# Kernel optimization log

Measured on AMD Instinct MI355X. Metric: run time of the kernel, lower is better.

Reference implementation:

```python
import jax, jax.numpy as jnp
import numpy as np

NUM_HEADS = 8
KERNEL = 7  # odd, dilation = 1


def _neighbor_indices(n, k):
    # NATTEN semantics: window start clamped so the kxk window stays inside [0, n)
    r = k // 2
    starts = jnp.clip(jnp.arange(n) - r, 0, n - k)  # [n]
    return starts[:, None] + jnp.arange(k)[None, :]  # [n, k]


def setup_inputs() -> dict:
    key = jax.random.key(0)
    k1, k2, k3, k4 = jax.random.split(key, 4)
    B, H, W, C = 2, 56, 56, 256
    return {
        "x": jax.random.normal(k1, (B, H, W, C), dtype=jnp.float32),
        "w_qk": jax.random.normal(k2, (2 * C, C), dtype=jnp.float32) * 0.02,
        "w_v": jax.random.normal(k3, (C, C), dtype=jnp.float32) * 0.02,
        "w_proj": jax.random.normal(k4, (C, C), dtype=jnp.float32) * 0.02,
        "b_proj": jnp.zeros((C,), dtype=jnp.float32),
    }


def reference(x, w_qk, w_v, w_proj, b_proj):
    B, H, W, C = x.shape
    NH, K = NUM_HEADS, KERNEL
    HD = C // NH
    scale = HD ** -0.5

    # qk / v projections (torch Linear: y = x @ W.T)
    qk = (x @ w_qk.T).reshape(B, H, W, 2, NH, HD)
    q = jnp.moveaxis(qk[:, :, :, 0], 3, 1) * scale  # [B, NH, H, W, HD]
    k = jnp.moveaxis(qk[:, :, :, 1], 3, 1)          # [B, NH, H, W, HD]
    v = jnp.moveaxis((x @ w_v.T).reshape(B, H, W, NH, HD), 3, 1)  # [B, NH, H, W, HD]

    idx_h = _neighbor_indices(H, K)  # [H, K]
    idx_w = _neighbor_indices(W, K)  # [W, K]
    ih = idx_h[:, None, :, None]  # [H, 1, K, 1]
    iw = idx_w[None, :, None, :]  # [1, W, 1, K]

    # Gather per-pixel neighborhoods: [B, NH, H, W, K, K, HD]
    k_nb = k[:, :, ih, iw, :]
    v_nb = v[:, :, ih, iw, :]

    # windowed QK^T -> [B, NH, H, W, K*K]
    attn = jnp.einsum('bnijf,bnijpqf->bnijpq', q, k_nb).reshape(B, NH, H, W, K * K)
    attn = jax.nn.softmax(attn, axis=-1)

    # windowed AV -> [B, NH, H, W, HD]
    out = jnp.einsum('bnijk,bnijkf->bnijf', attn, v_nb.reshape(B, NH, H, W, K * K, HD))

    out = jnp.moveaxis(out, 1, 3).reshape(B, H, W, C)
    out = out @ w_proj.T + b_proj
    return out, attn
```

## Files before the change

### kernel.cpp

```cpp
#include <hip/hip_runtime.h>
#include <math.h>

#define Bb   2
#define Hh   56
#define Ww   56
#define Cc   256
#define NHh  8
#define HDd  32
#define KK   7
#define HWsz (Hh*Ww)
#define Mtot (Bb*Hh*Ww)

typedef __bf16 bf16x8 __attribute__((ext_vector_type(8)));
typedef __bf16 bf16x4 __attribute__((ext_vector_type(4)));
typedef float  f32x4  __attribute__((ext_vector_type(4)));

__global__ __launch_bounds__(256) void gemm_qkv_f(
    const float* __restrict__ X, const float* __restrict__ Wqk,
    const float* __restrict__ Wv, __bf16* __restrict__ Out, float scale)
{
    __shared__ __bf16 As[4096];
    __shared__ __bf16 Bs[4096];

    const int Kdim = 256;
    const int tid = threadIdx.x;
    const int m0  = blockIdx.y * 64;
    const int n0  = blockIdx.x * 64;

    const int mm = tid >> 2;
    const int q  = tid & 3;
    const float* arow = X + (size_t)(m0 + mm) * Kdim + q * 16;
    const float* brow = (n0 < 512)
        ? (Wqk + (size_t)(n0 + mm) * Kdim + q * 16)
        : (Wv  + (size_t)(n0 + mm - 512) * Kdim + q * 16);

    const int ks_st  = q >> 1;
    const int sub_st = mm >> 4;
    const int row_st = mm & 15;
    const int c0_st  = (q & 1) * 2;
    const int blk_st = ks_st * 4 + sub_st;
    const int off0 = blk_st * 512 + row_st * 32 + ((c0_st ^ (row_st & 3)) * 8);
    const int off1 = blk_st * 512 + row_st * 32 + (((c0_st + 1) ^ (row_st & 3)) * 8);

    const int w    = tid >> 6;
    const int lane = tid & 63;
    const int fr_row = lane & 15;
    const int fr_c   = lane >> 4;
    const int fr_off = fr_row * 32 + ((fr_c ^ (fr_row & 3)) * 8);

    f32x4 acc[4] = {};

    for (int k0 = 0; k0 < Kdim; k0 += 64) {
        float4 a0 = *(const float4*)(arow + k0);
        float4 a1 = *(const float4*)(arow + k0 + 4);
        float4 a2 = *(const float4*)(arow + k0 + 8);
        float4 a3 = *(const float4*)(arow + k0 + 12);
        float4 b0 = *(const float4*)(brow + k0);
        float4 b1 = *(const float4*)(brow + k0 + 4);
        float4 b2 = *(const float4*)(brow + k0 + 8);
        float4 b3 = *(const float4*)(brow + k0 + 12);
        bf16x8 av0 = { (__bf16)a0.x, (__bf16)a0.y, (__bf16)a0.z, (__bf16)a0.w,
                       (__bf16)a1.x, (__bf16)a1.y, (__bf16)a1.z, (__bf16)a1.w };
        bf16x8 av1 = { (__bf16)a2.x, (__bf16)a2.y, (__bf16)a2.z, (__bf16)a2.w,
                       (__bf16)a3.x, (__bf16)a3.y, (__bf16)a3.z, (__bf16)a3.w };
        bf16x8 bv0 = { (__bf16)b0.x, (__bf16)b0.y, (__bf16)b0.z, (__bf16)b0.w,
                       (__bf16)b1.x, (__bf16)b1.y, (__bf16)b1.z, (__bf16)b1.w };
        bf16x8 bv1 = { (__bf16)b2.x, (__bf16)b2.y, (__bf16)b2.z, (__bf16)b2.w,
                       (__bf16)b3.x, (__bf16)b3.y, (__bf16)b3.z, (__bf16)b3.w };
        __syncthreads();
        *(bf16x8*)&As[off0] = av0;
        *(bf16x8*)&As[off1] = av1;
        *(bf16x8*)&Bs[off0] = bv0;
        *(bf16x8*)&Bs[off1] = bv1;
        __syncthreads();
        #pragma unroll
        for (int ks = 0; ks < 2; ++ks) {
            bf16x8 af = *(const bf16x8*)&As[(ks * 4 + w) * 512 + fr_off];
            #pragma unroll
            for (int n = 0; n < 4; ++n) {
                bf16x8 bfr = *(const bf16x8*)&Bs[(ks * 4 + n) * 512 + fr_off];
                acc[n] = __builtin_amdgcn_mfma_f32_16x16x32_bf16(af, bfr, acc[n], 0, 0, 0);
            }
        }
    }

    #pragma unroll
    for (int n = 0; n < 4; ++n) {
        const int gcol = n0 + n * 16 + fr_row;
        const float sc_ = (gcol < 256) ? scale : 1.f;
        #pragma unroll
        for (int r = 0; r < 4; ++r) {
            const int grow = m0 + w * 16 + fr_c * 4 + r;
            Out[(size_t)grow * 768 + gcol] = (__bf16)(acc[n][r] * sc_);
        }
    }
}

__global__ __launch_bounds__(256) void gemm_proj_f(
    const __bf16* __restrict__ A, const float* __restrict__ W,
    float* __restrict__ Cout, const float* __restrict__ bias)
{
    __shared__ __bf16 As[4096];
    __shared__ __bf16 Bs[4096];

    const int Kdim = 256, N = 256;
    const int tid = threadIdx.x;
    const int m0  = blockIdx.y * 64;
    const int n0  = blockIdx.x * 64;

    const int mm = tid >> 2;
    const int q  = tid & 3;
    const __bf16* arow = A + (size_t)(m0 + mm) * Kdim + q * 16;
    const float*  brow = W + (size_t)(n0 + mm) * Kdim + q * 16;

    const int ks_st  = q >> 1;
    const int sub_st = mm >> 4;
    const int row_st = mm & 15;
    const int c0_st  = (q & 1) * 2;
    const int blk_st = ks_st * 4 + sub_st;
    const int off0 = blk_st * 512 + row_st * 32 + ((c0_st ^ (row_st & 3)) * 8);
    const int off1 = blk_st * 512 + row_st * 32 + (((c0_st + 1) ^ (row_st & 3)) * 8);

    const int w    = tid >> 6;
    const int lane = tid & 63;
    const int fr_row = lane & 15;
    const int fr_c   = lane >> 4;
    const int fr_off = fr_row * 32 + ((fr_c ^ (fr_row & 3)) * 8);

    f32x4 acc[4] = {};

    for (int k0 = 0; k0 < Kdim; k0 += 64) {
        bf16x8 av0 = *(const bf16x8*)(arow + k0);
        bf16x8 av1 = *(const bf16x8*)(arow + k0 + 8);
        float4 b0 = *(const float4*)(brow + k0);
        float4 b1 = *(const float4*)(brow + k0 + 4);
        float4 b2 = *(const float4*)(brow + k0 + 8);
        float4 b3 = *(const float4*)(brow + k0 + 12);
        bf16x8 bv0 = { (__bf16)b0.x, (__bf16)b0.y, (__bf16)b0.z, (__bf16)b0.w,
                       (__bf16)b1.x, (__bf16)b1.y, (__bf16)b1.z, (__bf16)b1.w };
        bf16x8 bv1 = { (__bf16)b2.x, (__bf16)b2.y, (__bf16)b2.z, (__bf16)b2.w,
                       (__bf16)b3.x, (__bf16)b3.y, (__bf16)b3.z, (__bf16)b3.w };
        __syncthreads();
        *(bf16x8*)&As[off0] = av0;
        *(bf16x8*)&As[off1] = av1;
        *(bf16x8*)&Bs[off0] = bv0;
        *(bf16x8*)&Bs[off1] = bv1;
        __syncthreads();
        #pragma unroll
        for (int ks = 0; ks < 2; ++ks) {
            bf16x8 af = *(const bf16x8*)&As[(ks * 4 + w) * 512 + fr_off];
            #pragma unroll
            for (int n = 0; n < 4; ++n) {
                bf16x8 bfr = *(const bf16x8*)&Bs[(ks * 4 + n) * 512 + fr_off];
                acc[n] = __builtin_amdgcn_mfma_f32_16x16x32_bf16(af, bfr, acc[n], 0, 0, 0);
            }
        }
    }

    #pragma unroll
    for (int n = 0; n < 4; ++n) {
        const int gcol = n0 + n * 16 + fr_row;
        const float bs_ = bias[gcol];
        #pragma unroll
        for (int r = 0; r < 4; ++r) {
            const int grow = m0 + w * 16 + fr_c * 4 + r;
            Cout[(size_t)grow * N + gcol] = acc[n][r] + bs_;
        }
    }
}

__global__ __launch_bounds__(256, 5) void nattn_84(
    const __bf16* __restrict__ qkv, __bf16* __restrict__ attn_out,
    float* __restrict__ attn_glob)
{
    __shared__ __align__(16) __bf16 Ks[140 * 40];
    __shared__ float Ss[32 * 49];

    const int bx   = blockIdx.x;
    const int head = bx & 7;
    int t = bx >> 3;
    const int tj = t % 14; t /= 14;
    const int ti = t % 7;
    const int b  = t / 7;
    const int tid = threadIdx.x;

    int base_h = ti * 8 - 3; if (base_h < 0) base_h = 0; if (base_h > Hh - 14) base_h = Hh - 14;
    int base_w = tj * 4 - 3; if (base_w < 0) base_w = 0; if (base_w > Ww - 10) base_w = Ww - 10;

    const int pixb = b * HWsz;
    const int hoff = head * 32;

    #pragma unroll
    for (int it = 0; it < 3; ++it) {
        const int idx = tid + it * 256;
        if (idx < 560) {
            const int p = idx >> 2, c = idx & 3;
            const int pix = pixb + (base_h + p / 10) * Ww + base_w + p % 10;
            *(bf16x8*)&Ks[p * 40 + c * 8] =
                *(const bf16x8*)&qkv[(size_t)pix * 768 + 256 + hoff + c * 8];
        }
    }

    const int q  = tid >> 3;
    const int r  = tid & 7;
    const int qi = ti * 8 + (q >> 2);
    const int qj = tj * 4 + (q & 3);

    float qreg[32];
    {
        const __bf16* qp = &qkv[(size_t)(pixb + qi * Ww + qj) * 768 + hoff];
        #pragma unroll
        for (int c = 0; c < 4; ++c) {
            bf16x8 qv = *(const bf16x8*)(qp + c * 8);
            #pragma unroll
            for (int j = 0; j < 8; ++j) qreg[c * 8 + j] = (float)qv[j];
        }
    }

    bf16x8 vreg[3];
    #pragma unroll
    for (int it = 0; it < 3; ++it) {
        const int idx = tid + it * 256;
        if (idx < 560) {
            const int p = idx >> 2, c = idx & 3;
            const int pix = pixb + (base_h + p / 10) * Ww + base_w + p % 10;
            vreg[it] = *(const bf16x8*)&qkv[(size_t)pix * 768 + 512 + hoff + c * 8];
        }
    }
    __syncthreads();

    int ih0 = qi - 3; if (ih0 < 0) ih0 = 0; if (ih0 > Hh - 7) ih0 = Hh - 7;
    int iw0 = qj - 3; if (iw0 < 0) iw0 = 0; if (iw0 > Ww - 7) iw0 = Ww - 7;
    const int lh0 = ih0 - base_h, lw0 = iw0 - base_w;

    float sc[7];
    float mx = -1e30f;
    #pragma unroll
    for (int tt = 0; tt < 7; ++tt) {
        const int k = r + 8 * tt;
        if (k < 49) {
            const int krow = (lh0 + k / 7) * 10 + lw0 + k % 7;
            const __bf16* kp = &Ks[krow * 40];
            float acc = 0.f;
            #pragma unroll
            for (int c = 0; c < 4; ++c) {
                bf16x8 kv = *(const bf16x8*)(kp + c * 8);
                #pragma unroll
                for (int j = 0; j < 8; ++j)
                    acc += qreg[c * 8 + j] * (float)kv[j];
            }
            sc[tt] = acc;
            mx = fmaxf(mx, acc);
        }
    }
    mx = fmaxf(mx, __shfl_xor(mx, 1));
    mx = fmaxf(mx, __shfl_xor(mx, 2));
    mx = fmaxf(mx, __shfl_xor(mx, 4));
    float sum = 0.f;
    #pragma unroll
    for (int tt = 0; tt < 7; ++tt) {
        const int k = r + 8 * tt;
        if (k < 49) { sc[tt] = __expf(sc[tt] - mx); sum += sc[tt]; }
    }
    sum += __shfl_xor(sum, 1);
    sum += __shfl_xor(sum, 2);
    sum += __shfl_xor(sum, 4);
    const float inv = 1.f / sum;
    #pragma unroll
    for (int tt = 0; tt < 7; ++tt) {
        const int k = r + 8 * tt;
        if (k < 49) Ss[q * 49 + k] = sc[tt] * inv;
    }
    __syncthreads();

    #pragma unroll
    for (int it = 0; it < 3; ++it) {
        const int idx = tid + it * 256;
        if (idx < 560) {
            const int p = idx >> 2, c = idx & 3;
            *(bf16x8*)&Ks[p * 40 + c * 8] = vreg[it];
        }
    }
    const size_t agbase = (size_t)(b * NHh + head) * HWsz;
    for (int idx = tid; idx < 32 * 49; idx += 256) {
        const int qq = idx / 49, k = idx - qq * 49;
        attn_glob[(agbase + (ti * 8 + (qq >> 2)) * Ww + tj * 4 + (qq & 3)) * 49 + k]
            = Ss[qq * 49 + k];
    }
    __syncthreads();

    const int rc  = r & 3;
    const int par = r >> 2;
    float a[8] = {};
    #pragma unroll
    for (int tt = 0; tt < 25; ++tt) {
        const int k = par + 2 * tt;
        if (k < 49) {
            const float pr = Ss[q * 49 + k];
            const int vrow = (lh0 + k / 7) * 10 + lw0 + k % 7;
            bf16x8 v8 = *(const bf16x8*)&Ks[vrow * 40 + rc * 8];
            #pragma unroll
            for (int j = 0; j < 8; ++j)
                a[j] += pr * (float)v8[j];
        }
    }
    #pragma unroll
    for (int j = 0; j < 8; ++j) a[j] += __shfl_xor(a[j], 4);

    bf16x4 o = { (__bf16)a[par * 4 + 0], (__bf16)a[par * 4 + 1],
                 (__bf16)a[par * 4 + 2], (__bf16)a[par * 4 + 3] };
    *(bf16x4*)(attn_out + (size_t)(pixb + qi * Ww + qj) * 256 + hoff + rc * 8 + par * 4) = o;
}

extern "C" void kernel_launch(void* const* d_in, const int* in_sizes, int n_in,
                              void* d_out, int out_size, void* d_ws, size_t ws_size,
                              hipStream_t stream)
{
    const float* x      = (const float*)d_in[0];
    const float* w_qk   = (const float*)d_in[1];
    const float* w_v    = (const float*)d_in[2];
    const float* w_proj = (const float*)d_in[3];
    const float* b_proj = (const float*)d_in[4];

    float* out       = (float*)d_out;
    float* attn_glob = out + (size_t)Mtot * Cc;

    __bf16* qkv_ws  = (__bf16*)d_ws;
    __bf16* attn_ws = qkv_ws + (size_t)Mtot * 768;

    const float scale = 0.17677669529663687f;

    gemm_qkv_f<<<dim3(768 / 64, Mtot / 64), 256, 0, stream>>>(
        x, w_qk, w_v, qkv_ws, scale);

    nattn_84<<<Bb * 7 * 14 * NHh, 256, 0, stream>>>(qkv_ws, attn_ws, attn_glob);

    gemm_proj_f<<<dim3(256 / 64, Mtot / 64), 256, 0, stream>>>(
        attn_ws, w_proj, out, b_proj);
}
```

Baseline: 107.6 us.

## Pre-convert inputs and weights to bf16 and load full K-panel into LDS

Adds a prep kernel that converts x and all weight matrices to bf16 once, so the GEMMs read half-width data instead of converting fp32 on every tile load. Both GEMMs now stage the entire 256-deep K panel in shared memory with a single barrier and run the MFMA loop without per-step syncs. The cost is an extra launch, an extra fp32 read plus bf16 write of x, and 64KB of LDS per block, which lowers occupancy.

```diff
diff --git a/kernel.cpp b/kernel.cpp
--- a/kernel.cpp
+++ b/kernel.cpp
@@ -15,32 +15,52 @@
 typedef __bf16 bf16x4 __attribute__((ext_vector_type(4)));
 typedef float  f32x4  __attribute__((ext_vector_type(4)));
 
-__global__ __launch_bounds__(256) void gemm_qkv_f(
-    const float* __restrict__ X, const float* __restrict__ Wqk,
-    const float* __restrict__ Wv, __bf16* __restrict__ Out, float scale)
-{
-    __shared__ __bf16 As[4096];
-    __shared__ __bf16 Bs[4096];
-
-    const int Kdim = 256;
+__global__ __launch_bounds__(256) void prep_bf16(
+    const float* __restrict__ x, const float* __restrict__ wqk,
+    const float* __restrict__ wv, const float* __restrict__ wp,
+    __bf16* __restrict__ xb, __bf16* __restrict__ wallb, __bf16* __restrict__ wpb)
+{
+    const int t = blockIdx.x * 256 + threadIdx.x;
+    const float* src; __bf16* dst; int off;
+    if (t < 200704)      { src = x;   dst = xb;             off = t; }
+    else if (t < 217088) { src = wqk; dst = wallb;          off = t - 200704; }
+    else if (t < 225280) { src = wv;  dst = wallb + 131072; off = t - 217088; }
+    else                 { src = wp;  dst = wpb;            off = t - 225280; }
+    const int e = off * 8;
+    float4 a = *(const float4*)(src + e);
+    float4 b = *(const float4*)(src + e + 4);
+    bf16x8 o = { (__bf16)a.x, (__bf16)a.y, (__bf16)a.z, (__bf16)a.w,
+                 (__bf16)b.x, (__bf16)b.y, (__bf16)b.z, (__bf16)b.w };
+    *(bf16x8*)(dst + e) = o;
+}
+
+__global__ __launch_bounds__(256) void gemm_qkv_p(
+    const __bf16* __restrict__ A, const __bf16* __restrict__ Wall,
+    __bf16* __restrict__ Out, float scale)
+{
+    __shared__ __bf16 As[16384];
+    __shared__ __bf16 Bs[16384];
+
     const int tid = threadIdx.x;
     const int m0  = blockIdx.y * 64;
     const int n0  = blockIdx.x * 64;
 
-    const int mm = tid >> 2;
-    const int q  = tid & 3;
-    const float* arow = X + (size_t)(m0 + mm) * Kdim + q * 16;
-    const float* brow = (n0 < 512)
-        ? (Wqk + (size_t)(n0 + mm) * Kdim + q * 16)
-        : (Wv  + (size_t)(n0 + mm - 512) * Kdim + q * 16);
-
-    const int ks_st  = q >> 1;
-    const int sub_st = mm >> 4;
-    const int row_st = mm & 15;
-    const int c0_st  = (q & 1) * 2;
-    const int blk_st = ks_st * 4 + sub_st;
-    const int off0 = blk_st * 512 + row_st * 32 + ((c0_st ^ (row_st & 3)) * 8);
-    const int off1 = blk_st * 512 + row_st * 32 + (((c0_st + 1) ^ (row_st & 3)) * 8);
+    const int mm  = tid >> 2;
+    const int q   = tid & 3;
+    const int sub = mm >> 4;
+    const int row = mm & 15;
+    const __bf16* arow = A    + (size_t)(m0 + mm) * 256 + q * 64;
+    const __bf16* brow = Wall + (size_t)(n0 + mm) * 256 + q * 64;
+
+    #pragma unroll
+    for (int i = 0; i < 8; ++i) {
+        const int ks  = q * 2 + (i >> 2);
+        const int c   = i & 3;
+        const int off = (ks * 4 + sub) * 512 + row * 32 + ((c ^ (row & 3)) * 8);
+        *(bf16x8*)&As[off] = *(const bf16x8*)(arow + i * 8);
+        *(bf16x8*)&Bs[off] = *(const bf16x8*)(brow + i * 8);
+    }
+    __syncthreads();
 
     const int w    = tid >> 6;
     const int lane = tid & 63;
@@ -49,38 +69,13 @@
     const int fr_off = fr_row * 32 + ((fr_c ^ (fr_row & 3)) * 8);
 
     f32x4 acc[4] = {};
-
-    for (int k0 = 0; k0 < Kdim; k0 += 64) {
-        float4 a0 = *(const float4*)(arow + k0);
-        float4 a1 = *(const float4*)(arow + k0 + 4);
-        float4 a2 = *(const float4*)(arow + k0 + 8);
-        float4 a3 = *(const float4*)(arow + k0 + 12);
-        float4 b0 = *(const float4*)(brow + k0);
-        float4 b1 = *(const float4*)(brow + k0 + 4);
-        float4 b2 = *(const float4*)(brow + k0 + 8);
-        float4 b3 = *(const float4*)(brow + k0 + 12);
-        bf16x8 av0 = { (__bf16)a0.x, (__bf16)a0.y, (__bf16)a0.z, (__bf16)a0.w,
-                       (__bf16)a1.x, (__bf16)a1.y, (__bf16)a1.z, (__bf16)a1.w };
-        bf16x8 av1 = { (__bf16)a2.x, (__bf16)a2.y, (__bf16)a2.z, (__bf16)a2.w,
-                       (__bf16)a3.x, (__bf16)a3.y, (__bf16)a3.z, (__bf16)a3.w };
-        bf16x8 bv0 = { (__bf16)b0.x, (__bf16)b0.y, (__bf16)b0.z, (__bf16)b0.w,
-                       (__bf16)b1.x, (__bf16)b1.y, (__bf16)b1.z, (__bf16)b1.w };
-        bf16x8 bv1 = { (__bf16)b2.x, (__bf16)b2.y, (__bf16)b2.z, (__bf16)b2.w,
-                       (__bf16)b3.x, (__bf16)b3.y, (__bf16)b3.z, (__bf16)b3.w };
-        __syncthreads();
-        *(bf16x8*)&As[off0] = av0;
-        *(bf16x8*)&As[off1] = av1;
-        *(bf16x8*)&Bs[off0] = bv0;
-        *(bf16x8*)&Bs[off1] = bv1;
-        __syncthreads();
-        #pragma unroll
-        for (int ks = 0; ks < 2; ++ks) {
-            bf16x8 af = *(const bf16x8*)&As[(ks * 4 + w) * 512 + fr_off];
-            #pragma unroll
-            for (int n = 0; n < 4; ++n) {
-                bf16x8 bfr = *(const bf16x8*)&Bs[(ks * 4 + n) * 512 + fr_off];
-                acc[n] = __builtin_amdgcn_mfma_f32_16x16x32_bf16(af, bfr, acc[n], 0, 0, 0);
-            }
+    #pragma unroll
+    for (int ks = 0; ks < 8; ++ks) {
+        bf16x8 af = *(const bf16x8*)&As[(ks * 4 + w) * 512 + fr_off];
+        #pragma unroll
+        for (int n = 0; n < 4; ++n) {
+            bf16x8 bfr = *(const bf16x8*)&Bs[(ks * 4 + n) * 512 + fr_off];
+            acc[n] = __builtin_amdgcn_mfma_f32_16x16x32_bf16(af, bfr, acc[n], 0, 0, 0);
         }
     }
 
@@ -96,30 +91,34 @@
     }
 }
 
-__global__ __launch_bounds__(256) void gemm_proj_f(
-    const __bf16* __restrict__ A, const float* __restrict__ W,
+__global__ __launch_bounds__(256) void gemm_proj_p(
+    const __bf16* __restrict__ A, const __bf16* __restrict__ W,
     float* __restrict__ Cout, const float* __restrict__ bias)
 {
-    __shared__ __bf16 As[4096];
-    __shared__ __bf16 Bs[4096];
-
-    const int Kdim = 256, N = 256;
+    __shared__ __bf16 As[16384];
+    __shared__ __bf16 Bs[16384];
+
+    const int N = 256;
     const int tid = threadIdx.x;
     const int m0  = blockIdx.y * 64;
     const int n0  = blockIdx.x * 64;
 
-    const int mm = tid >> 2;
-    const int q  = tid & 3;
-    const __bf16* arow = A + (size_t)(m0 + mm) * Kdim + q * 16;
-    const float*  brow = W + (size_t)(n0 + mm) * Kdim + q * 16;
-
-    const int ks_st  = q >> 1;
-    const int sub_st = mm >> 4;
-    const int row_st = mm & 15;
-    const int c0_st  = (q & 1) * 2;
-    const int blk_st = ks_st * 4 + sub_st;
-    const int off0 = blk_st * 512 + row_st * 32 + ((c0_st ^ (row_st & 3)) * 8);
-    const int off1 = blk_st * 512 + row_st * 32 + (((c0_st + 1) ^ (row_st & 3)) * 8);
+    const int mm  = tid >> 2;
+    const int q   = tid & 3;
+    const int sub = mm >> 4;
+    const int row = mm & 15;
+    const __bf16* arow = A + (size_t)(m0 + mm) * 256 + q * 64;
+    const __bf16* brow = W + (size_t)(n0 + mm) * 256 + q * 64;
+
+    #pragma unroll
+    for (int i = 0; i < 8; ++i) {
+        const int ks  = q * 2 + (i >> 2);
+        const int c   = i & 3;
+        const int off = (ks * 4 + sub) * 512 + row * 32 + ((c ^ (row & 3)) * 8);
+        *(bf16x8*)&As[off] = *(const bf16x8*)(arow + i * 8);
+        *(bf16x8*)&Bs[off] = *(const bf16x8*)(brow + i * 8);
+    }
+    __syncthreads();
 
     const int w    = tid >> 6;
     const int lane = tid & 63;
@@ -128,32 +127,13 @@
     const int fr_off = fr_row * 32 + ((fr_c ^ (fr_row & 3)) * 8);
 
     f32x4 acc[4] = {};
-
-    for (int k0 = 0; k0 < Kdim; k0 += 64) {
-        bf16x8 av0 = *(const bf16x8*)(arow + k0);
-        bf16x8 av1 = *(const bf16x8*)(arow + k0 + 8);
-        float4 b0 = *(const float4*)(brow + k0);
-        float4 b1 = *(const float4*)(brow + k0 + 4);
-        float4 b2 = *(const float4*)(brow + k0 + 8);
-        float4 b3 = *(const float4*)(brow + k0 + 12);
-        bf16x8 bv0 = { (__bf16)b0.x, (__bf16)b0.y, (__bf16)b0.z, (__bf16)b0.w,
-                       (__bf16)b1.x, (__bf16)b1.y, (__bf16)b1.z, (__bf16)b1.w };
-        bf16x8 bv1 = { (__bf16)b2.x, (__bf16)b2.y, (__bf16)b2.z, (__bf16)b2.w,
-                       (__bf16)b3.x, (__bf16)b3.y, (__bf16)b3.z, (__bf16)b3.w };
-        __syncthreads();
-        *(bf16x8*)&As[off0] = av0;
-        *(bf16x8*)&As[off1] = av1;
-        *(bf16x8*)&Bs[off0] = bv0;
-        *(bf16x8*)&Bs[off1] = bv1;
-        __syncthreads();
-        #pragma unroll
-        for (int ks = 0; ks < 2; ++ks) {
-            bf16x8 af = *(const bf16x8*)&As[(ks * 4 + w) * 512 + fr_off];
-            #pragma unroll
-            for (int n = 0; n < 4; ++n) {
-                bf16x8 bfr = *(const bf16x8*)&Bs[(ks * 4 + n) * 512 + fr_off];
-                acc[n] = __builtin_amdgcn_mfma_f32_16x16x32_bf16(af, bfr, acc[n], 0, 0, 0);
-            }
+    #pragma unroll
+    for (int ks = 0; ks < 8; ++ks) {
+        bf16x8 af = *(const bf16x8*)&As[(ks * 4 + w) * 512 + fr_off];
+        #pragma unroll
+        for (int n = 0; n < 4; ++n) {
+            bf16x8 bfr = *(const bf16x8*)&Bs[(ks * 4 + n) * 512 + fr_off];
+            acc[n] = __builtin_amdgcn_mfma_f32_16x16x32_bf16(af, bfr, acc[n], 0, 0, 0);
         }
     }
 
@@ -325,16 +305,21 @@
     float* out       = (float*)d_out;
     float* attn_glob = out + (size_t)Mtot * Cc;
 
-    __bf16* qkv_ws  = (__bf16*)d_ws;
+    __bf16* xb      = (__bf16*)d_ws;
+    __bf16* wallb   = xb + (size_t)Mtot * 256;
+    __bf16* wpb     = wallb + 768 * 256;
+    __bf16* qkv_ws  = wpb + 256 * 256;
     __bf16* attn_ws = qkv_ws + (size_t)Mtot * 768;
 
     const float scale = 0.17677669529663687f;
 
-    gemm_qkv_f<<<dim3(768 / 64, Mtot / 64), 256, 0, stream>>>(
-        x, w_qk, w_v, qkv_ws, scale);
+    prep_bf16<<<912, 256, 0, stream>>>(x, w_qk, w_v, w_proj, xb, wallb, wpb);
+
+    gemm_qkv_p<<<dim3(768 / 64, Mtot / 64), 256, 0, stream>>>(
+        xb, wallb, qkv_ws, scale);
 
     nattn_84<<<Bb * 7 * 14 * NHh, 256, 0, stream>>>(qkv_ws, attn_ws, attn_glob);
 
-    gemm_proj_f<<<dim3(256 / 64, Mtot / 64), 256, 0, stream>>>(
-        attn_ws, w_proj, out, b_proj);
-}
+    gemm_proj_p<<<dim3(256 / 64, Mtot / 64), 256, 0, stream>>>(
+        attn_ws, wpb, out, b_proj);
+}
```

After: 111.0 us. 3.2% more time.

## Pre-convert inputs and weights to bf16 and swizzle block order across XCDs

Applied to the files above, without the earlier changes.

Adds a prep kernel that converts x and all weight matrices to bf16 once, so both GEMMs load bf16 directly instead of re-reading and converting fp32 tiles in every block. It also remaps block indices in all three kernels so consecutive blocks are spread across the 8 XCDs in contiguous chunks, aiming at better L2 locality. This adds a kernel launch and an extra write and read of x in bf16, and the weights are re-converted on every call.

```diff
diff --git a/kernel.cpp b/kernel.cpp
--- a/kernel.cpp
+++ b/kernel.cpp
@@ -15,24 +15,43 @@
 typedef __bf16 bf16x4 __attribute__((ext_vector_type(4)));
 typedef float  f32x4  __attribute__((ext_vector_type(4)));
 
-__global__ __launch_bounds__(256) void gemm_qkv_f(
-    const float* __restrict__ X, const float* __restrict__ Wqk,
-    const float* __restrict__ Wv, __bf16* __restrict__ Out, float scale)
+__global__ __launch_bounds__(256) void prep_bf16(
+    const float* __restrict__ x, const float* __restrict__ wqk,
+    const float* __restrict__ wv, const float* __restrict__ wp,
+    __bf16* __restrict__ xb, __bf16* __restrict__ wallb, __bf16* __restrict__ wpb)
+{
+    const int t = blockIdx.x * 256 + threadIdx.x;
+    const float* src; __bf16* dst; int off;
+    if (t < 200704)      { src = x;   dst = xb;             off = t; }
+    else if (t < 217088) { src = wqk; dst = wallb;          off = t - 200704; }
+    else if (t < 225280) { src = wv;  dst = wallb + 131072; off = t - 217088; }
+    else                 { src = wp;  dst = wpb;            off = t - 225280; }
+    const int e = off * 8;
+    float4 a = *(const float4*)(src + e);
+    float4 b = *(const float4*)(src + e + 4);
+    bf16x8 o = { (__bf16)a.x, (__bf16)a.y, (__bf16)a.z, (__bf16)a.w,
+                 (__bf16)b.x, (__bf16)b.y, (__bf16)b.z, (__bf16)b.w };
+    *(bf16x8*)(dst + e) = o;
+}
+
+__global__ __launch_bounds__(256) void gemm_qkv_b(
+    const __bf16* __restrict__ A, const __bf16* __restrict__ Wall,
+    __bf16* __restrict__ Out, float scale)
 {
     __shared__ __bf16 As[4096];
     __shared__ __bf16 Bs[4096];
 
     const int Kdim = 256;
     const int tid = threadIdx.x;
-    const int m0  = blockIdx.y * 64;
-    const int n0  = blockIdx.x * 64;
+    const int bid = blockIdx.x;
+    const int swz = (bid & 7) * 147 + (bid >> 3);
+    const int m0  = (swz / 12) * 64;
+    const int n0  = (swz % 12) * 64;
 
     const int mm = tid >> 2;
     const int q  = tid & 3;
-    const float* arow = X + (size_t)(m0 + mm) * Kdim + q * 16;
-    const float* brow = (n0 < 512)
-        ? (Wqk + (size_t)(n0 + mm) * Kdim + q * 16)
-        : (Wv  + (size_t)(n0 + mm - 512) * Kdim + q * 16);
+    const __bf16* arow = A    + (size_t)(m0 + mm) * Kdim + q * 16;
+    const __bf16* brow = Wall + (size_t)(n0 + mm) * Kdim + q * 16;
 
     const int ks_st  = q >> 1;
     const int sub_st = mm >> 4;
@@ -51,22 +70,10 @@
     f32x4 acc[4] = {};
 
     for (int k0 = 0; k0 < Kdim; k0 += 64) {
-        float4 a0 = *(const float4*)(arow + k0);
-        float4 a1 = *(const float4*)(arow + k0 + 4);
-        float4 a2 = *(const float4*)(arow + k0 + 8);
-        float4 a3 = *(const float4*)(arow + k0 + 12);
-        float4 b0 = *(const float4*)(brow + k0);
-        float4 b1 = *(const float4*)(brow + k0 + 4);
-        float4 b2 = *(const float4*)(brow + k0 + 8);
-        float4 b3 = *(const float4*)(brow + k0 + 12);
-        bf16x8 av0 = { (__bf16)a0.x, (__bf16)a0.y, (__bf16)a0.z, (__bf16)a0.w,
-                       (__bf16)a1.x, (__bf16)a1.y, (__bf16)a1.z, (__bf16)a1.w };
-        bf16x8 av1 = { (__bf16)a2.x, (__bf16)a2.y, (__bf16)a2.z, (__bf16)a2.w,
-                       (__bf16)a3.x, (__bf16)a3.y, (__bf16)a3.z, (__bf16)a3.w };
-        bf16x8 bv0 = { (__bf16)b0.x, (__bf16)b0.y, (__bf16)b0.z, (__bf16)b0.w,
-                       (__bf16)b1.x, (__bf16)b1.y, (__bf16)b1.z, (__bf16)b1.w };
-        bf16x8 bv1 = { (__bf16)b2.x, (__bf16)b2.y, (__bf16)b2.z, (__bf16)b2.w,
-                       (__bf16)b3.x, (__bf16)b3.y, (__bf16)b3.z, (__bf16)b3.w };
+        bf16x8 av0 = *(const bf16x8*)(arow + k0);
+        bf16x8 av1 = *(const bf16x8*)(arow + k0 + 8);
+        bf16x8 bv0 = *(const bf16x8*)(brow + k0);
+        bf16x8 bv1 = *(const bf16x8*)(brow + k0 + 8);
         __syncthreads();
         *(bf16x8*)&As[off0] = av0;
         *(bf16x8*)&As[off1] = av1;
@@ -96,8 +103,8 @@
     }
 }
 
-__global__ __launch_bounds__(256) void gemm_proj_f(
-    const __bf16* __restrict__ A, const float* __restrict__ W,
+__global__ __launch_bounds__(256) void gemm_proj_b(
+    const __bf16* __restrict__ A, const __bf16* __restrict__ W,
     float* __restrict__ Cout, const float* __restrict__ bias)
 {
     __shared__ __bf16 As[4096];
@@ -105,13 +112,15 @@
 
     const int Kdim = 256, N = 256;
     const int tid = threadIdx.x;
-    const int m0  = blockIdx.y * 64;
-    const int n0  = blockIdx.x * 64;
+    const int bid = blockIdx.x;
+    const int swz = (bid & 7) * 49 + (bid >> 3);
+    const int m0  = (swz / 4) * 64;
+    const int n0  = (swz % 4) * 64;
 
     const int mm = tid >> 2;
     const int q  = tid & 3;
     const __bf16* arow = A + (size_t)(m0 + mm) * Kdim + q * 16;
-    const float*  brow = W + (size_t)(n0 + mm) * Kdim + q * 16;
+    const __bf16* brow = W + (size_t)(n0 + mm) * Kdim + q * 16;
 
     const int ks_st  = q >> 1;
     const int sub_st = mm >> 4;
@@ -132,14 +141,8 @@
     for (int k0 = 0; k0 < Kdim; k0 += 64) {
         bf16x8 av0 = *(const bf16x8*)(arow + k0);
         bf16x8 av1 = *(const bf16x8*)(arow + k0 + 8);
-        float4 b0 = *(const float4*)(brow + k0);
-        float4 b1 = *(const float4*)(brow + k0 + 4);
-        float4 b2 = *(const float4*)(brow + k0 + 8);
-        float4 b3 = *(const float4*)(brow + k0 + 12);
-        bf16x8 bv0 = { (__bf16)b0.x, (__bf16)b0.y, (__bf16)b0.z, (__bf16)b0.w,
-                       (__bf16)b1.x, (__bf16)b1.y, (__bf16)b1.z, (__bf16)b1.w };
-        bf16x8 bv1 = { (__bf16)b2.x, (__bf16)b2.y, (__bf16)b2.z, (__bf16)b2.w,
-                       (__bf16)b3.x, (__bf16)b3.y, (__bf16)b3.z, (__bf16)b3.w };
+        bf16x8 bv0 = *(const bf16x8*)(brow + k0);
+        bf16x8 bv1 = *(const bf16x8*)(brow + k0 + 8);
         __syncthreads();
         *(bf16x8*)&As[off0] = av0;
         *(bf16x8*)&As[off1] = av1;
@@ -176,9 +179,10 @@
     __shared__ __align__(16) __bf16 Ks[140 * 40];
     __shared__ float Ss[32 * 49];
 
-    const int bx   = blockIdx.x;
-    const int head = bx & 7;
-    int t = bx >> 3;
+    const int bid = blockIdx.x;
+    const int swz = (bid & 7) * 196 + (bid >> 3);
+    const int head = swz & 7;
+    int t = swz >> 3;
     const int tj = t % 14; t /= 14;
     const int ti = t % 7;
     const int b  = t / 7;
@@ -325,16 +329,19 @@
     float* out       = (float*)d_out;
     float* attn_glob = out + (size_t)Mtot * Cc;
 
-    __bf16* qkv_ws  = (__bf16*)d_ws;
+    __bf16* xb      = (__bf16*)d_ws;
+    __bf16* wallb   = xb + (size_t)Mtot * 256;
+    __bf16* wpb     = wallb + 768 * 256;
+    __bf16* qkv_ws  = wpb + 256 * 256;
     __bf16* attn_ws = qkv_ws + (size_t)Mtot * 768;
 
     const float scale = 0.17677669529663687f;
 
-    gemm_qkv_f<<<dim3(768 / 64, Mtot / 64), 256, 0, stream>>>(
-        x, w_qk, w_v, qkv_ws, scale);
+    prep_bf16<<<912, 256, 0, stream>>>(x, w_qk, w_v, w_proj, xb, wallb, wpb);
+
+    gemm_qkv_b<<<1176, 256, 0, stream>>>(xb, wallb, qkv_ws, scale);
 
     nattn_84<<<Bb * 7 * 14 * NHh, 256, 0, stream>>>(qkv_ws, attn_ws, attn_glob);
 
-    gemm_proj_f<<<dim3(256 / 64, Mtot / 64), 256, 0, stream>>>(
-        attn_ws, w_proj, out, b_proj);
-}
+    gemm_proj_b<<<392, 256, 0, stream>>>(attn_ws, wpb, out, b_proj);
+}
```

Measured after the change: 106.2 us. About the same (-1.3%).
